# Kernel tuning notes

Measured on AMD Instinct MI355X. Metric: run time of the kernel, lower is better.

Reference implementation:

```python
import jax, jax.numpy as jnp
import numpy as np

PAD = 10      # padding_length (hardcoded in module)
CS = 128      # cell_size
A = -0.75     # PyTorch bicubic convolution constant


def _cubic_weights(t):
    """PyTorch bicubic (Keys, a=-0.75) weights for offsets [-1,0,1,2], t in [0,1)."""
    t2 = t * t
    t3 = t2 * t
    w0 = A * (t3 - 2.0 * t2 + t)
    w1 = (A + 2.0) * t3 - (A + 3.0) * t2 + 1.0
    s = 1.0 - t
    s2 = s * s
    s3 = s2 * s
    w2 = (A + 2.0) * s3 - (A + 3.0) * s2 + 1.0
    w3 = A * (s3 - 2.0 * s2 + s)
    return (w0, w1, w2, w3)


def setup_inputs() -> dict:
    key = jax.random.key(0)
    k1, k2 = jax.random.split(key)
    H, W = 4000, 4000
    n0 = -(-H // CS)
    n1 = -(-W // CS)
    N = n0 * n1  # 1024
    matrix = jax.random.normal(k1, (H, W), dtype=jnp.float32)
    ident = jnp.tile(jnp.array([[1.0, 0.0, 0.0], [0.0, 1.0, 0.0]], dtype=jnp.float32), (N, 1, 1))
    theta = ident + 0.02 * jax.random.normal(k2, (N, 2, 3), dtype=jnp.float32)
    return {"matrix": matrix, "theta": theta}


def reference(matrix, theta):
    H, W = matrix.shape
    csp = CS + 2 * PAD                       # padded cell size = 148
    n0 = -(-H // CS)
    n1 = -(-W // CS)
    N = n0 * n1

    # manual zero pad (PAD each side) + unfold's implicit PAD each side -> 2*PAD
    padded = jnp.pad(matrix, ((2 * PAD, CS - H % CS + 2 * PAD),
                              (2 * PAD, CS - W % CS + 2 * PAD)))

    # unfold: tiles of size csp with stride CS, row-major over (n0, n1)
    idx0 = jnp.arange(n0)[:, None] * CS + jnp.arange(csp)[None, :]  # (n0, csp)
    idx1 = jnp.arange(n1)[:, None] * CS + jnp.arange(csp)[None, :]  # (n1, csp)
    tiles = padded[idx0[:, :, None, None], idx1[None, None, :, :]]  # (n0, csp, n1, csp)
    tiles = tiles.transpose(0, 2, 1, 3).reshape(N, csp, csp)

    # affine_grid, align_corners=False: base coords x_j = (2j+1)/size - 1
    base = (2.0 * jnp.arange(csp, dtype=matrix.dtype) + 1.0) / csp - 1.0
    xs = base[None, None, :]
    ys = base[None, :, None]
    gx = theta[:, 0, 0, None, None] * xs + theta[:, 0, 1, None, None] * ys + theta[:, 0, 2, None, None]
    gy = theta[:, 1, 0, None, None] * xs + theta[:, 1, 1, None, None] * ys + theta[:, 1, 2, None, None]

    # grid_sample unnormalize (align_corners=False)
    ix = ((gx + 1.0) * csp - 1.0) * 0.5
    iy = ((gy + 1.0) * csp - 1.0) * 0.5
    ix0 = jnp.floor(ix)
    tx = ix - ix0
    ix0 = ix0.astype(jnp.int32)
    iy0 = jnp.floor(iy)
    ty = iy - iy0
    iy0 = iy0.astype(jnp.int32)
    wx = _cubic_weights(tx)
    wy = _cubic_weights(ty)

    bidx = jnp.arange(N)[:, None, None]
    out = jnp.zeros_like(ix)
    for ky in range(4):  # fixed 4x4 bicubic stencil
        row = iy0 - 1 + ky
        rv = (row >= 0) & (row < csp)
        rc = jnp.clip(row, 0, csp - 1)
        for kx in range(4):
            col = ix0 - 1 + kx
            cv = (col >= 0) & (col < csp)
            cc = jnp.clip(col, 0, csp - 1)
            v = tiles[bidx, rc, cc]
            out = out + wy[ky] * wx[kx] * jnp.where(rv & cv, v, jnp.zeros_like(v))

    # crop interior CSxCS of each cell and reassemble
    inner = out[:, PAD:PAD + CS, PAD:PAD + CS].reshape(n0, n1, CS, CS)
    full = inner.transpose(0, 2, 1, 3).reshape(n0 * CS, n1 * CS)
    return full[:H, :W]
```

## Files before the change

kernel.cpp:

```cpp
#include <hip/hip_runtime.h>

#define PAD 10
#define CS 128
#define CSP 148
#define AH 4000
#define AW 4000
#define RPT 8
#define BROWS 16
#define NTILES 1024
#define NBANDS 8
#define NBLK (NTILES*NBANDS)

#define PREPG(S, IXF, IYF)                                                    \
    do {                                                                      \
        const float fx0_ = floorf(IXF), fy0_ = floorf(IYF);                   \
        txs[S] = (IXF) - fx0_; tys[S] = (IYF) - fy0_;                         \
        const int ixi_ = (int)fx0_, iyi_ = (int)fy0_;                         \
        ixis[S] = ixi_; iyis[S] = iyi_;                                       \
        fasts[S] = (ixi_ - 1 >= lo_c) & (ixi_ + 2 <= hi_c) &                  \
                   (iyi_ - 1 >= lo_r) & (iyi_ + 2 <= hi_r);                   \
        int mr_ = gr0 + iyi_ - 1; mr_ = mr_ < 0 ? 0 : (mr_ > AH-4 ? AH-4 : mr_); \
        int mc_ = gc0 + ixi_ - 1; mc_ = mc_ < 0 ? 0 : (mc_ > AW-4 ? AW-4 : mc_); \
        const float* p_ = matrix + (size_t)mr_ * AW + mc_;                    \
        __builtin_memcpy(&qg[S][0], p_,        16);                           \
        __builtin_memcpy(&qg[S][1], p_ + AW,   16);                           \
        __builtin_memcpy(&qg[S][2], p_ + 2*AW, 16);                           \
        __builtin_memcpy(&qg[S][3], p_ + 3*AW, 16);                           \
    } while (0)

__global__ __launch_bounds__(256) void shift_bicubic_kernel(
    const float* __restrict__ matrix,
    const float* __restrict__ theta,
    float* __restrict__ out)
{
    const int bid  = blockIdx.x;
    const int sid  = (bid & 7) * (NBLK/8) + (bid >> 3);
    const int tile = sid >> 3;
    const int band = sid & 7;
    const int i0   = tile >> 5;
    const int i1   = tile & 31;
    const int c    = threadIdx.x & 127;
    const int sub  = threadIdx.x >> 7;
    const int rb   = band * BROWS;
    const int r0   = rb + sub*RPT;
    const int w    = i1*CS + c;
    const int h0   = i0*CS + r0;
    if (w >= AW || h0 >= AH) return;

    const float t00 = theta[tile*6+0], t01 = theta[tile*6+1], t02 = theta[tile*6+2];
    const float t10 = theta[tile*6+3], t11 = theta[tile*6+4], t12 = theta[tile*6+5];

    const float xs  = (2.0f*(float)(c + PAD) + 1.0f) * (1.0f/148.0f) - 1.0f;
    const float ys0 = (2.0f*(float)(r0 + PAD) + 1.0f) * (1.0f/148.0f) - 1.0f;
    const float bx  = fmaf(t00, xs, t02);
    const float by  = fmaf(t10, xs, t12);
    const float ixf0 = fmaf(fmaf(t01, ys0, bx), 74.0f, 73.5f);
    const float iyf0 = fmaf(fmaf(t11, ys0, by), 74.0f, 73.5f);

    const int gr0 = i0*CS - 2*PAD;
    const int gc0 = i1*CS - 2*PAD;
    const int lo_c = (gc0 < 0) ? -gc0 : 0;
    const int hi_c = (gc0 + CSP - 1 > AW - 1) ? (AW - 1 - gc0) : (CSP - 1);
    const int lo_r = (gr0 < 0) ? -gr0 : 0;
    const int hi_r = (gr0 + CSP - 1 > AH - 1) ? (AH - 1 - gr0) : (CSP - 1);

    float  txs[2], tys[2];
    int    ixis[2], iyis[2];
    bool   fasts[2];
    float4 qg[2][4];

    PREPG(0, ixf0, iyf0);

    int oidx = h0*AW + w;
    #pragma unroll
    for (int k = 0; k < RPT; ++k) {
        if (k + 1 < RPT) {
            const float ixfn = fmaf((float)(k+1), t01, ixf0);
            const float iyfn = fmaf((float)(k+1), t11, iyf0);
            PREPG((k+1)&1, ixfn, iyfn);
        }
        __builtin_amdgcn_sched_barrier(0);

        const int   S  = k & 1;
        const float tx = txs[S], ty = tys[S];
        const float A_ = -0.75f, AP2 = 1.25f, mAP3 = -2.25f;
        const float sx = 1.0f - tx, sy = 1.0f - ty;
        const float tx2 = tx*tx, sx2 = sx*sx;
        const float ty2 = ty*ty, sy2 = sy*sy;
        const float wx0 = A_*(tx*sx2);
        const float wx3 = A_*(sx*tx2);
        const float wx1 = fmaf(tx2, fmaf(AP2, tx, mAP3), 1.0f);
        const float wx2 = fmaf(sx2, fmaf(AP2, sx, mAP3), 1.0f);
        const float wy0 = A_*(ty*sy2);
        const float wy3 = A_*(sy*ty2);
        const float wy1 = fmaf(ty2, fmaf(AP2, ty, mAP3), 1.0f);
        const float wy2 = fmaf(sy2, fmaf(AP2, sy, mAP3), 1.0f);

        float acc;
        if (fasts[S]) {
            const float4 q0 = qg[S][0], q1 = qg[S][1], q2 = qg[S][2], q3 = qg[S][3];
            const float a0 = fmaf(wx3,q0.w, fmaf(wx2,q0.z, fmaf(wx1,q0.y, wx0*q0.x)));
            const float a1 = fmaf(wx3,q1.w, fmaf(wx2,q1.z, fmaf(wx1,q1.y, wx0*q1.x)));
            const float a2 = fmaf(wx3,q2.w, fmaf(wx2,q2.z, fmaf(wx1,q2.y, wx0*q2.x)));
            const float a3 = fmaf(wx3,q3.w, fmaf(wx2,q3.z, fmaf(wx1,q3.y, wx0*q3.x)));
            acc = fmaf(wy3,a3, fmaf(wy2,a2, fmaf(wy1,a1, wy0*a0)));
        } else {
            const float wxa[4] = {wx0, wx1, wx2, wx3};
            const float wya[4] = {wy0, wy1, wy2, wy3};
            const int ixi = ixis[S], iyi = iyis[S];
            acc = 0.0f;
            #pragma unroll
            for (int ky = 0; ky < 4; ++ky) {
                const int row = iyi - 1 + ky;
                const int gr  = gr0 + row;
                const bool rok = (row >= 0) & (row < CSP) & (gr >= 0) & (gr < AH);
                float racc = 0.0f;
                #pragma unroll
                for (int kx = 0; kx < 4; ++kx) {
                    const int col = ixi - 1 + kx;
                    const int gc  = gc0 + col;
                    const bool cok = rok & (col >= 0) & (col < CSP) & (gc >= 0) & (gc < AW);
                    const float v = cok ? matrix[(size_t)gr*AW + gc] : 0.0f;
                    racc = fmaf(wxa[kx], v, racc);
                }
                acc = fmaf(wya[ky], racc, acc);
            }
        }
        if (h0 + k < AH) __builtin_nontemporal_store(acc, &out[oidx]);
        oidx += AW;
    }
}

extern "C" void kernel_launch(void* const* d_in, const int* in_sizes, int n_in,
                              void* d_out, int out_size, void* d_ws, size_t ws_size,
                              hipStream_t stream) {
    const float* matrix = (const float*)d_in[0];
    const float* theta  = (const float*)d_in[1];
    float* out = (float*)d_out;

    dim3 block(256, 1, 1);
    dim3 grid(NBLK, 1, 1);
    shift_bicubic_kernel<<<grid, block, 0, stream>>>(matrix, theta, out);
}
```

Before: 43.19 us.

## Reuse stencil rows across output rows with a rolling register window

Adds a per-block interior check that tests the affine-mapped corners of the block's region; when all samples are interior, each thread keeps a 5-entry ring of float4 rows and loads only one new row per output row, instead of four. If the integer sample position shifts differently than expected, the three missing rows are reloaded. Rows per thread double to 16 and bands per tile drop to 4, which halves the block count and adds register pressure. The old per-row gather path remains as a fallback for blocks near the boundary.

Result: slower. 46.31 us (+7.2%).

```diff
diff --git a/kernel.cpp b/kernel.cpp
--- a/kernel.cpp
+++ b/kernel.cpp
@@ -5,11 +5,16 @@
 #define CSP 148
 #define AH 4000
 #define AW 4000
-#define RPT 8
-#define BROWS 16
-#define NTILES 1024
-#define NBANDS 8
-#define NBLK (NTILES*NBANDS)
+#define RPT 16
+#define BROWS 32
+#define NBANDS 4
+#define NBLK (1024*NBANDS)
+
+#define LDROW(DST, ROWL, COLL)                                                \
+    do {                                                                      \
+        const int off_ = (gr0 + (ROWL))*AW + (gc0 + (COLL));                  \
+        __builtin_memcpy(&(DST), matrix + off_, 16);                          \
+    } while (0)
 
 #define PREPG(S, IXF, IYF)                                                    \
     do {                                                                      \
@@ -35,8 +40,8 @@
 {
     const int bid  = blockIdx.x;
     const int sid  = (bid & 7) * (NBLK/8) + (bid >> 3);
-    const int tile = sid >> 3;
-    const int band = sid & 7;
+    const int tile = sid >> 2;
+    const int band = sid & 3;
     const int i0   = tile >> 5;
     const int i1   = tile & 31;
     const int c    = threadIdx.x & 127;
@@ -64,70 +69,156 @@
     const int lo_r = (gr0 < 0) ? -gr0 : 0;
     const int hi_r = (gr0 + CSP - 1 > AH - 1) ? (AH - 1 - gr0) : (CSP - 1);
 
-    float  txs[2], tys[2];
-    int    ixis[2], iyis[2];
-    bool   fasts[2];
-    float4 qg[2][4];
-
-    PREPG(0, ixf0, iyf0);
+    const int cact = (AW - 1 - i1*CS < CS - 1) ? (AW - 1 - i1*CS) : (CS - 1);
+    const int ract = (rb + BROWS - 1 < AH - 1 - i0*CS) ? (rb + BROWS - 1)
+                                                       : (AH - 1 - i0*CS);
+    const float xsA = (2.0f*(float)(PAD)        + 1.0f)*(1.0f/148.0f) - 1.0f;
+    const float xsB = (2.0f*(float)(cact + PAD) + 1.0f)*(1.0f/148.0f) - 1.0f;
+    const float ysA = (2.0f*(float)(rb   + PAD) + 1.0f)*(1.0f/148.0f) - 1.0f;
+    const float ysB = (2.0f*(float)(ract + PAD) + 1.0f)*(1.0f/148.0f) - 1.0f;
+    const float ixAA = fmaf(fmaf(t01, ysA, fmaf(t00, xsA, t02)), 74.0f, 73.5f);
+    const float ixAB = fmaf(fmaf(t01, ysB, fmaf(t00, xsA, t02)), 74.0f, 73.5f);
+    const float ixBA = fmaf(fmaf(t01, ysA, fmaf(t00, xsB, t02)), 74.0f, 73.5f);
+    const float ixBB = fmaf(fmaf(t01, ysB, fmaf(t00, xsB, t02)), 74.0f, 73.5f);
+    const float iyAA = fmaf(fmaf(t11, ysA, fmaf(t10, xsA, t12)), 74.0f, 73.5f);
+    const float iyAB = fmaf(fmaf(t11, ysB, fmaf(t10, xsA, t12)), 74.0f, 73.5f);
+    const float iyBA = fmaf(fmaf(t11, ysA, fmaf(t10, xsB, t12)), 74.0f, 73.5f);
+    const float iyBB = fmaf(fmaf(t11, ysB, fmaf(t10, xsB, t12)), 74.0f, 73.5f);
+    const float ixmn = fminf(fminf(ixAA, ixAB), fminf(ixBA, ixBB));
+    const float ixmx = fmaxf(fmaxf(ixAA, ixAB), fmaxf(ixBA, ixBB));
+    const float iymn = fminf(fminf(iyAA, iyAB), fminf(iyBA, iyBB));
+    const float iymx = fmaxf(fmaxf(iyAA, iyAB), fmaxf(iyBA, iyBB));
+    const bool allfast =
+        (ixmn >= (float)(lo_c + 1) + 0.01f) & (ixmx <= (float)(hi_c - 1) - 0.01f) &
+        (iymn >= (float)(lo_r + 1) + 0.01f) & (iymx <= (float)(hi_r - 1) - 0.01f);
 
     int oidx = h0*AW + w;
-    #pragma unroll
-    for (int k = 0; k < RPT; ++k) {
-        if (k + 1 < RPT) {
-            const float ixfn = fmaf((float)(k+1), t01, ixf0);
-            const float iyfn = fmaf((float)(k+1), t11, iyf0);
-            PREPG((k+1)&1, ixfn, iyfn);
+
+    if (allfast) {
+        float4 R[5];
+        float ptx, pty;
+        int   pixi, piyi;
+        {
+            const float fx = floorf(ixf0), fy = floorf(iyf0);
+            ptx = ixf0 - fx;  pty = iyf0 - fy;
+            pixi = (int)fx;   piyi = (int)fy;
+            LDROW(R[0], piyi-1, pixi-1);
+            LDROW(R[1], piyi,   pixi-1);
+            LDROW(R[2], piyi+1, pixi-1);
+            LDROW(R[3], piyi+2, pixi-1);
         }
-        __builtin_amdgcn_sched_barrier(0);
-
-        const int   S  = k & 1;
-        const float tx = txs[S], ty = tys[S];
-        const float A_ = -0.75f, AP2 = 1.25f, mAP3 = -2.25f;
-        const float sx = 1.0f - tx, sy = 1.0f - ty;
-        const float tx2 = tx*tx, sx2 = sx*sx;
-        const float ty2 = ty*ty, sy2 = sy*sy;
-        const float wx0 = A_*(tx*sx2);
-        const float wx3 = A_*(sx*tx2);
-        const float wx1 = fmaf(tx2, fmaf(AP2, tx, mAP3), 1.0f);
-        const float wx2 = fmaf(sx2, fmaf(AP2, sx, mAP3), 1.0f);
-        const float wy0 = A_*(ty*sy2);
-        const float wy3 = A_*(sy*ty2);
-        const float wy1 = fmaf(ty2, fmaf(AP2, ty, mAP3), 1.0f);
-        const float wy2 = fmaf(sy2, fmaf(AP2, sy, mAP3), 1.0f);
-
-        float acc;
-        if (fasts[S]) {
-            const float4 q0 = qg[S][0], q1 = qg[S][1], q2 = qg[S][2], q3 = qg[S][3];
-            const float a0 = fmaf(wx3,q0.w, fmaf(wx2,q0.z, fmaf(wx1,q0.y, wx0*q0.x)));
-            const float a1 = fmaf(wx3,q1.w, fmaf(wx2,q1.z, fmaf(wx1,q1.y, wx0*q1.x)));
-            const float a2 = fmaf(wx3,q2.w, fmaf(wx2,q2.z, fmaf(wx1,q2.y, wx0*q2.x)));
-            const float a3 = fmaf(wx3,q3.w, fmaf(wx2,q3.z, fmaf(wx1,q3.y, wx0*q3.x)));
-            acc = fmaf(wy3,a3, fmaf(wy2,a2, fmaf(wy1,a1, wy0*a0)));
-        } else {
-            const float wxa[4] = {wx0, wx1, wx2, wx3};
-            const float wya[4] = {wy0, wy1, wy2, wy3};
-            const int ixi = ixis[S], iyi = iyis[S];
-            acc = 0.0f;
-            #pragma unroll
-            for (int ky = 0; ky < 4; ++ky) {
-                const int row = iyi - 1 + ky;
-                const int gr  = gr0 + row;
-                const bool rok = (row >= 0) & (row < CSP) & (gr >= 0) & (gr < AH);
-                float racc = 0.0f;
+        #pragma unroll
+        for (int k = 0; k < RPT; ++k) {
+            float ntx = 0.0f, nty = 0.0f;
+            int   nxi = 0, nyi = 0;
+            bool  shiftOK = true;
+            if (k + 1 < RPT) {
+                const float ixf = fmaf((float)(k+1), t01, ixf0);
+                const float iyf = fmaf((float)(k+1), t11, iyf0);
+                const float fx = floorf(ixf), fy = floorf(iyf);
+                ntx = ixf - fx;  nty = iyf - fy;
+                nxi = (int)fx;   nyi = (int)fy;
+                shiftOK = (nxi == pixi) & (nyi == piyi + 1);
+                LDROW(R[(k+4)%5], nyi+2, nxi-1);
+            }
+            __builtin_amdgcn_sched_barrier(0);
+
+            {
+                const float txk = ptx, tyk = pty;
+                const float A_ = -0.75f, AP2 = 1.25f, mAP3 = -2.25f;
+                const float sx = 1.0f - txk, sy = 1.0f - tyk;
+                const float tx2 = txk*txk, sx2 = sx*sx;
+                const float ty2 = tyk*tyk, sy2 = sy*sy;
+                const float wx0 = A_*(txk*sx2);
+                const float wx3 = A_*(sx*tx2);
+                const float wx1 = fmaf(tx2, fmaf(AP2, txk, mAP3), 1.0f);
+                const float wx2 = fmaf(sx2, fmaf(AP2, sx, mAP3), 1.0f);
+                const float wy0 = A_*(tyk*sy2);
+                const float wy3 = A_*(sy*ty2);
+                const float wy1 = fmaf(ty2, fmaf(AP2, tyk, mAP3), 1.0f);
+                const float wy2 = fmaf(sy2, fmaf(AP2, sy, mAP3), 1.0f);
+                const float4 q0 = R[(k+0)%5], q1 = R[(k+1)%5];
+                const float4 q2 = R[(k+2)%5], q3 = R[(k+3)%5];
+                const float a0 = fmaf(wx3,q0.w, fmaf(wx2,q0.z, fmaf(wx1,q0.y, wx0*q0.x)));
+                const float a1 = fmaf(wx3,q1.w, fmaf(wx2,q1.z, fmaf(wx1,q1.y, wx0*q1.x)));
+                const float a2 = fmaf(wx3,q2.w, fmaf(wx2,q2.z, fmaf(wx1,q2.y, wx0*q2.x)));
+                const float a3 = fmaf(wx3,q3.w, fmaf(wx2,q3.z, fmaf(wx1,q3.y, wx0*q3.x)));
+                const float acc = fmaf(wy3,a3, fmaf(wy2,a2, fmaf(wy1,a1, wy0*a0)));
+                __builtin_nontemporal_store(acc, &out[oidx]);
+                oidx += AW;
+            }
+
+            if (k + 1 < RPT) {
+                if (!shiftOK) {
+                    LDROW(R[(k+1)%5], nyi-1, nxi-1);
+                    LDROW(R[(k+2)%5], nyi,   nxi-1);
+                    LDROW(R[(k+3)%5], nyi+1, nxi-1);
+                }
+                pixi = nxi; piyi = nyi; ptx = ntx; pty = nty;
+            }
+        }
+    } else {
+        float  txs[2], tys[2];
+        int    ixis[2], iyis[2];
+        bool   fasts[2];
+        float4 qg[2][4];
+        PREPG(0, ixf0, iyf0);
+        #pragma unroll
+        for (int k = 0; k < RPT; ++k) {
+            if (k + 1 < RPT) {
+                const float ixfn = fmaf((float)(k+1), t01, ixf0);
+                const float iyfn = fmaf((float)(k+1), t11, iyf0);
+                PREPG((k+1)&1, ixfn, iyfn);
+            }
+            __builtin_amdgcn_sched_barrier(0);
+            const int   S  = k & 1;
+            const float tx = txs[S], ty = tys[S];
+            const float A_ = -0.75f, AP2 = 1.25f, mAP3 = -2.25f;
+            const float sx = 1.0f - tx, sy = 1.0f - ty;
+            const float tx2 = tx*tx, sx2 = sx*sx;
+            const float ty2 = ty*ty, sy2 = sy*sy;
+            const float wx0 = A_*(tx*sx2);
+            const float wx3 = A_*(sx*tx2);
+            const float wx1 = fmaf(tx2, fmaf(AP2, tx, mAP3), 1.0f);
+            const float wx2 = fmaf(sx2, fmaf(AP2, sx, mAP3), 1.0f);
+            const float wy0 = A_*(ty*sy2);
+            const float wy3 = A_*(sy*ty2);
+            const float wy1 = fmaf(ty2, fmaf(AP2, ty, mAP3), 1.0f);
+            const float wy2 = fmaf(sy2, fmaf(AP2, sy, mAP3), 1.0f);
+
+            float acc;
+            if (fasts[S]) {
+                const float4 q0 = qg[S][0], q1 = qg[S][1], q2 = qg[S][2], q3 = qg[S][3];
+                const float a0 = fmaf(wx3,q0.w, fmaf(wx2,q0.z, fmaf(wx1,q0.y, wx0*q0.x)));
+                const float a1 = fmaf(wx3,q1.w, fmaf(wx2,q1.z, fmaf(wx1,q1.y, wx0*q1.x)));
+                const float a2 = fmaf(wx3,q2.w, fmaf(wx2,q2.z, fmaf(wx1,q2.y, wx0*q2.x)));
+                const float a3 = fmaf(wx3,q3.w, fmaf(wx2,q3.z, fmaf(wx1,q3.y, wx0*q3.x)));
+                acc = fmaf(wy3,a3, fmaf(wy2,a2, fmaf(wy1,a1, wy0*a0)));
+            } else {
+                const float wxa[4] = {wx0, wx1, wx2, wx3};
+                const float wya[4] = {wy0, wy1, wy2, wy3};
+                const int ixi = ixis[S], iyi = iyis[S];
+                acc = 0.0f;
                 #pragma unroll
-                for (int kx = 0; kx < 4; ++kx) {
-                    const int col = ixi - 1 + kx;
-                    const int gc  = gc0 + col;
-                    const bool cok = rok & (col >= 0) & (col < CSP) & (gc >= 0) & (gc < AW);
-                    const float v = cok ? matrix[(size_t)gr*AW + gc] : 0.0f;
-                    racc = fmaf(wxa[kx], v, racc);
+                for (int ky = 0; ky < 4; ++ky) {
+                    const int row = iyi - 1 + ky;
+                    const int gr  = gr0 + row;
+                    const bool rok = (row >= 0) & (row < CSP) & (gr >= 0) & (gr < AH);
+                    float racc = 0.0f;
+                    #pragma unroll
+                    for (int kx = 0; kx < 4; ++kx) {
+                        const int col = ixi - 1 + kx;
+                        const int gc  = gc0 + col;
+                        const bool cok = rok & (col >= 0) & (col < CSP) & (gc >= 0) & (gc < AW);
+                        const float v = cok ? matrix[(size_t)gr*AW + gc] : 0.0f;
+                        racc = fmaf(wxa[kx], v, racc);
+                    }
+                    acc = fmaf(wya[ky], racc, acc);
                 }
-                acc = fmaf(wya[ky], racc, acc);
-            }
+            }
+            if (h0 + k < AH) __builtin_nontemporal_store(acc, &out[oidx]);
+            oidx += AW;
         }
-        if (h0 + k < AH) __builtin_nontemporal_store(acc, &out[oidx]);
-        oidx += AW;
     }
 }
 
```
